# Performance work log

Hardware: AMD Instinct MI355X
Metric: run time of the kernel (lower is better)

## Reference

```python
import jax, jax.numpy as jnp
import numpy as np

N_NODES = 10000
N_EDGES = 160000
MUL0 = 128   # multiplicity of 0e in node input/output
MUL1 = 64    # multiplicity of 1o in node input/output
FC_IN = 8    # radial basis size (edge_scalar_attr dim)
FC_H = 64    # fc_neurons = [64, 64]
NUM_NEIGHBORS = 16.0
ANGLE = np.pi / 8.0
MID0 = MUL0 + MUL1   # 192 scalars in irreps_mid (simplified)
MID1 = MUL0 + MUL1   # 192 vectors (1o) in irreps_mid


def _inv_sqrt(d):
    return 1.0 / np.sqrt(d)


def setup_inputs() -> dict:
    key = jax.random.key(0)
    ks = jax.random.split(key, 18)
    rn = lambda k, shape: jax.random.normal(k, shape, dtype=jnp.float32)
    inp = {
        'node_input': rn(ks[0], (N_NODES, MUL0 + 3 * MUL1)),
        'edge_attr': rn(ks[1], (N_EDGES, 4)),            # 1x0e + 1x1o spherical harmonics
        'edge_scalar_attr': rn(ks[2], (N_EDGES, FC_IN)),
        # first Linear: node_input -> (node_features || node_self_out)
        'Wa0': rn(ks[3], (MUL0, MUL0)),   # 0e -> 0e (message branch)
        'Wa1': rn(ks[4], (MUL1, MUL1)),   # 1o -> 1o (message branch)
        'Wb0': rn(ks[5], (MUL0, MUL0)),   # 0e -> 0e (self branch)
        'Wb1': rn(ks[6], (MUL1, MUL1)),   # 1o -> 1o (self branch)
        # radial MLP
        'M1': rn(ks[7], (FC_IN, FC_H)),
        'M2': rn(ks[8], (FC_H, FC_H)),
        # per-instruction TP weight generators: [FC_H, mul] ('uvu', v=1 squeezed)
        'Wtp0': rn(ks[9], (FC_H, MUL0)),   # 0e x 0e -> 0e
        'Wtp1': rn(ks[10], (FC_H, MUL0)),  # 0e x 1o -> 1o
        'Wtp2': rn(ks[11], (FC_H, MUL1)),  # 1o x 0e -> 1o
        'Wtp3': rn(ks[12], (FC_H, MUL1)),  # 1o x 1o -> 0e
        # output Linear: irreps_mid (192x0e + 192x1o) -> 128x0e + 64x1o
        'Wo0': rn(ks[13], (MID0, MUL0)),
        'Wo1': rn(ks[14], (MID1, MUL1)),
        'edge_src': jax.random.randint(ks[15], (N_EDGES,), 0, N_NODES),
        'edge_dst': jax.random.randint(ks[16], (N_EDGES,), 0, N_NODES),
    }
    return inp


def _forward(node_input, edge_attr, edge_scalar_attr,
             Wa0, Wa1, Wb0, Wb1, M1, M2,
             Wtp0, Wtp1, Wtp2, Wtp3, Wo0, Wo1,
             edge_src, edge_dst):
    n = node_input.shape[0]
    x0 = node_input[:, :MUL0]                         # [N,128] 0e
    x1 = node_input[:, MUL0:].reshape(n, MUL1, 3)     # [N,64,3] 1o

    # Linear(node_input.irreps + irreps_node_output): split into message / self
    feat0 = (x0 @ Wa0) * _inv_sqrt(MUL0)
    feat1 = jnp.einsum('nvi,vu->nui', x1, Wa1) * _inv_sqrt(MUL1)
    self0 = (x0 @ Wb0) * _inv_sqrt(MUL0)
    self1 = jnp.einsum('nvi,vu->nui', x1, Wb1) * _inv_sqrt(MUL1)

    # gather node features to edges
    e0 = feat0[edge_src]                              # [E,128]
    e1 = feat1[edge_src]                              # [E,64,3]
    y0 = edge_attr[:, 0:1]                            # [E,1] 0e
    y1 = edge_attr[:, 1:4]                            # [E,3] 1o

    # radial MLP -> per-edge per-path 'uvu' weights (path param / sqrt(fc_out))
    h = jax.nn.gelu(edge_scalar_attr @ M1 * _inv_sqrt(FC_IN))
    h = jax.nn.gelu(h @ M2 * _inv_sqrt(FC_H))
    w0 = h @ Wtp0 * _inv_sqrt(FC_H)                   # [E,128]
    w1 = h @ Wtp1 * _inv_sqrt(FC_H)                   # [E,128]
    w2 = h @ Wtp2 * _inv_sqrt(FC_H)                   # [E,64]
    w3 = h @ Wtp3 * _inv_sqrt(FC_H)                   # [E,64]

    # CG tensor product paths (component normalization: alpha = sqrt(dim_out))
    mid0a = w0 * e0 * y0                                        # 0e x 0e -> 0e [E,128]
    mid0b = w3 * jnp.einsum('eui,ei->eu', e1, y1) * _inv_sqrt(3.0)  # 1o.1o -> 0e [E,64]
    mid1a = w1[:, :, None] * e0[:, :, None] * y1[:, None, :]   # 0e x 1o -> 1o [E,128,3]
    mid1b = w2[:, :, None] * e1 * y0[:, :, None]                # 1o x 0e -> 1o [E,64,3]

    e_cnt = edge_attr.shape[0]
    edge_mid = jnp.concatenate(
        [mid0a, mid0b, mid1a.reshape(e_cnt, -1), mid1b.reshape(e_cnt, -1)], axis=1)  # [E,768]

    # scatter-add to destination nodes, divide by sqrt(num_neighbors)
    agg = jax.ops.segment_sum(edge_mid, edge_dst, num_segments=n) * _inv_sqrt(NUM_NEIGHBORS)

    z0 = agg[:, :MID0]                                          # [N,192] 0e
    z1 = jnp.concatenate(
        [agg[:, MID0:MID0 + 3 * MUL0].reshape(n, MUL0, 3),
         agg[:, MID0 + 3 * MUL0:].reshape(n, MUL1, 3)], axis=1)  # [N,192,3] 1o

    conv0 = (z0 @ Wo0) * _inv_sqrt(MID0)
    conv1 = jnp.einsum('nvi,vu->nui', z1, Wo1) * _inv_sqrt(MID1)

    c = np.cos(ANGLE).astype(np.float32)
    s = np.sin(ANGLE).astype(np.float32)
    out0 = c * self0 + s * conv0                                 # [N,128]
    out1 = c * self1 + s * conv1                                 # [N,64,3]
    return jnp.concatenate([out0, out1.reshape(n, -1)], axis=1)  # [N,320]


def reference(node_input, edge_attr, edge_scalar_attr,
              Wa0, Wa1, Wb0, Wb1, M1, M2,
              Wtp0, Wtp1, Wtp2, Wtp3, Wo0, Wo1,
              edge_src, edge_dst):
    return _forward(node_input, edge_attr, edge_scalar_attr,
                    Wa0, Wa1, Wb0, Wb1, M1, M2,
                    Wtp0, Wtp1, Wtp2, Wtp3, Wo0, Wo1,
                    edge_src, edge_dst)
```

## Files before the change

### kernel.cpp

```cpp
#include <hip/hip_runtime.h>
#include <hip/hip_bf16.h>
#include <hip/hip_fp16.h>

#define N_NODES 10000
#define N_EDGES 160000
#define FEAT_W 320
#define CHUNK 32

typedef _Float16 half8 __attribute__((ext_vector_type(8)));
typedef float f32x4 __attribute__((ext_vector_type(4)));

__device__ __forceinline__ float gelu_tanh(float x) {
    float x3 = x * x * x;
    float t = tanhf(0.7978845608028654f * (x + 0.044715f * x3));
    return 0.5f * x * (1.0f + t);
}

__global__ __launch_bounds__(320) void node_transform(
    const float* __restrict__ node_input,
    const float* __restrict__ Wa0, const float* __restrict__ Wa1,
    const float* __restrict__ Wb0, const float* __restrict__ Wb1,
    float* __restrict__ feat_tbl, float* __restrict__ self_tbl)
{
    __shared__ __align__(16) float xT[FEAT_W][8];
    const int node0 = blockIdx.x * 8;
    const int t = threadIdx.x;
    for (int q = t; q < 640; q += 320) {
        const int n = q / 80, c4 = q - n * 80;
        const float4 v = ((const float4*)(node_input + (size_t)(node0 + n) * FEAT_W))[c4];
        xT[c4 * 4 + 0][n] = v.x; xT[c4 * 4 + 1][n] = v.y;
        xT[c4 * 4 + 2][n] = v.z; xT[c4 * 4 + 3][n] = v.w;
    }
    __syncthreads();

    float accf[8] = {0,0,0,0,0,0,0,0}, accs[8] = {0,0,0,0,0,0,0,0};
    float scale;
    if (t < 128) {
        for (int v = 0; v < 128; ++v) {
            const float wa = Wa0[v * 128 + t];
            const float wb = Wb0[v * 128 + t];
            const float4 xa = *(const float4*)&xT[v][0];
            const float4 xb = *(const float4*)&xT[v][4];
            accf[0] += xa.x * wa; accf[1] += xa.y * wa; accf[2] += xa.z * wa; accf[3] += xa.w * wa;
            accf[4] += xb.x * wa; accf[5] += xb.y * wa; accf[6] += xb.z * wa; accf[7] += xb.w * wa;
            accs[0] += xa.x * wb; accs[1] += xa.y * wb; accs[2] += xa.z * wb; accs[3] += xa.w * wb;
            accs[4] += xb.x * wb; accs[5] += xb.y * wb; accs[6] += xb.z * wb; accs[7] += xb.w * wb;
        }
        scale = 0.08838834764831845f;
    } else {
        const int r = t - 128, u = r / 3, i = r - 3 * u;
        for (int v = 0; v < 64; ++v) {
            const float wa = Wa1[v * 64 + u];
            const float wb = Wb1[v * 64 + u];
            const int row = 128 + v * 3 + i;
            const float4 xa = *(const float4*)&xT[row][0];
            const float4 xb = *(const float4*)&xT[row][4];
            accf[0] += xa.x * wa; accf[1] += xa.y * wa; accf[2] += xa.z * wa; accf[3] += xa.w * wa;
            accf[4] += xb.x * wa; accf[5] += xb.y * wa; accf[6] += xb.z * wa; accf[7] += xb.w * wa;
            accs[0] += xa.x * wb; accs[1] += xa.y * wb; accs[2] += xa.z * wb; accs[3] += xa.w * wb;
            accs[4] += xb.x * wb; accs[5] += xb.y * wb; accs[6] += xb.z * wb; accs[7] += xb.w * wb;
        }
        scale = 0.125f;
    }
#pragma unroll
    for (int n = 0; n < 8; ++n) {
        feat_tbl[(size_t)(node0 + n) * FEAT_W + t] = accf[n] * scale;
        self_tbl[(size_t)(node0 + n) * FEAT_W + t] = accs[n] * scale;
    }
}

__global__ __launch_bounds__(256) void mlp_kernel(
    const float* __restrict__ esa,
    const float* __restrict__ M1,
    const float* __restrict__ M2,
    const int* __restrict__ edge_dst,
    __half* __restrict__ h2buf,
    int* __restrict__ counts)
{
    __shared__ __align__(16) float sh[4][64];
    const int wave = threadIdx.x >> 6;
    const int lane = threadIdx.x & 63;
    const int e = blockIdx.x * 4 + wave;

    if (lane == 0) atomicAdd(&counts[edge_dst[e]], 1);

    const float4 e0 = ((const float4*)(esa + (size_t)e * 8))[0];
    const float4 e1 = ((const float4*)(esa + (size_t)e * 8))[1];
    float h = e0.x * M1[0 * 64 + lane] + e0.y * M1[1 * 64 + lane]
            + e0.z * M1[2 * 64 + lane] + e0.w * M1[3 * 64 + lane]
            + e1.x * M1[4 * 64 + lane] + e1.y * M1[5 * 64 + lane]
            + e1.z * M1[6 * 64 + lane] + e1.w * M1[7 * 64 + lane];
    h = gelu_tanh(h * 0.35355339059327373f);
    sh[wave][lane] = h;
    __syncthreads();

    float h2 = 0.f;
    const float4* shp = (const float4*)sh[wave];
#pragma unroll
    for (int q = 0; q < 16; ++q) {
        const float4 s = shp[q];
        h2 += s.x * M2[(4 * q + 0) * 64 + lane];
        h2 += s.y * M2[(4 * q + 1) * 64 + lane];
        h2 += s.z * M2[(4 * q + 2) * 64 + lane];
        h2 += s.w * M2[(4 * q + 3) * 64 + lane];
    }
    h2 = gelu_tanh(h2 * 0.125f);
    h2buf[(size_t)e * 64 + lane] = (__half)(h2 * 0.125f);
}

__global__ __launch_bounds__(256) void pack_wtp(
    const float* __restrict__ Wtp0, const float* __restrict__ Wtp1,
    const float* __restrict__ Wtp2, const float* __restrict__ Wtp3,
    __half* __restrict__ wtp_pack)
{
    const int gid = blockIdx.x * 256 + threadIdx.x;
    if (gid >= 24 * 64) return;
    const int lane = gid & 63;
    const int tile = gid >> 6;
    const int quad = lane >> 4, n16 = lane & 15;
    const int col = tile * 16 + n16;
    const float* src; int stride;
    if (col < 128)      { src = Wtp0 + col;         stride = 128; }
    else if (col < 256) { src = Wtp1 + (col - 128); stride = 128; }
    else if (col < 320) { src = Wtp2 + (col - 256); stride = 64;  }
    else                { src = Wtp3 + (col - 320); stride = 64;  }
    __half* dst = wtp_pack + (size_t)gid * 16;
#pragma unroll
    for (int s = 0; s < 2; ++s)
#pragma unroll
        for (int j = 0; j < 8; ++j)
            dst[s * 8 + j] = (__half)src[(s * 32 + quad * 8 + j) * stride];
}

__global__ __launch_bounds__(1024) void scan_kernel(
    const int* __restrict__ counts, int* __restrict__ offsets, int* __restrict__ cursor)
{
    __shared__ int wsum[16];
    const int wid = threadIdx.x >> 6, lane = threadIdx.x & 63;
    int base = 0;
    for (int c = 0; c < 10; ++c) {
        const int i = c * 1024 + threadIdx.x;
        const int v = (i < N_NODES) ? counts[i] : 0;
        int x = v;
#pragma unroll
        for (int off = 1; off < 64; off <<= 1) {
            int y = __shfl_up(x, off, 64);
            if (lane >= off) x += y;
        }
        if (lane == 63) wsum[wid] = x;
        __syncthreads();
        if (threadIdx.x < 16) {
            int s = wsum[threadIdx.x];
#pragma unroll
            for (int off = 1; off < 16; off <<= 1) {
                int y = __shfl_up(s, off, 64);
                if ((int)threadIdx.x >= off) s += y;
            }
            wsum[threadIdx.x] = s;
        }
        __syncthreads();
        const int waveoff = (wid == 0) ? 0 : wsum[wid - 1];
        const int excl = base + waveoff + x - v;
        if (i < N_NODES) { offsets[i] = excl; cursor[i] = excl; }
        const int tot = wsum[15];
        __syncthreads();
        base += tot;
    }
    if (threadIdx.x == 0) offsets[N_NODES] = base;
}

__global__ void fill_kernel(const int* __restrict__ edge_dst,
                            const int* __restrict__ edge_src,
                            const float* __restrict__ edge_attr,
                            int* __restrict__ cursor, int* __restrict__ elist,
                            int* __restrict__ srcs_csr, float* __restrict__ y4csr) {
    int e = blockIdx.x * 256 + threadIdx.x;
    if (e < N_EDGES) {
        int pos = atomicAdd(&cursor[edge_dst[e]], 1);
        elist[pos] = e;
        srcs_csr[pos] = edge_src[e];
        ((float4*)y4csr)[pos] = ((const float4*)edge_attr)[e];
    }
}

__global__ __launch_bounds__(384) void gather_kernel(
    const int* __restrict__ offsets,
    const int* __restrict__ elist,
    const int* __restrict__ srcs_csr,
    const float* __restrict__ y4csr,
    const __half* __restrict__ h2buf,
    const __half* __restrict__ wtp_pack,
    const float* __restrict__ feat_tbl,
    const float* __restrict__ self_tbl,
    const float* __restrict__ Wo0,
    const float* __restrict__ Wo1,
    float* __restrict__ out)
{
    __shared__ __align__(16) __half wsh[CHUNK * 384];
    __shared__ __align__(16) __half h2s[CHUNK * 64];
    __shared__ float ys[CHUNK][4];
    __shared__ int   srcs[CHUNK];
    __shared__ float z[768];

    const int node = blockIdx.x;
    const int t = threadIdx.x;
    const int wave = t >> 6, lane = t & 63;
    const int quad = lane >> 4, n16 = lane & 15;

    half8 bf[4][2];
#pragma unroll
    for (int c = 0; c < 4; ++c) {
        const __half* p = wtp_pack + (size_t)((wave * 4 + c) * 64 + lane) * 16;
        bf[c][0] = *(const half8*)p;
        bf[c][1] = *(const half8*)(p + 8);
    }

    int f0;
    if (t < 128)      f0 = t;
    else if (t < 256) f0 = t - 128;
    else if (t < 320) f0 = 128 + 3 * (t - 256);
    else              f0 = 128 + 3 * (t - 320);

    float acc = 0.f, acc3a = 0.f, acc3b = 0.f, acc3c = 0.f;
    const int beg = offsets[node], end = offsets[node + 1];

    for (int cb = beg; cb < end; cb += CHUNK) {
        const int ne = min(CHUNK, end - cb);
        if (t < ne) {
            srcs[t] = srcs_csr[cb + t];
            ((float4*)ys)[t] = ((const float4*)y4csr)[cb + t];
        }
        for (int q = t; q < ne * 8; q += 384) {
            const int eL = q >> 3, u = q & 7;
            const half8 hv = ((const half8*)(h2buf + (size_t)elist[cb + eL] * 64))[u];
            *(half8*)((char*)h2s + eL * 128 + ((u * 16) ^ ((eL & 7) << 4))) = hv;
        }
        __syncthreads();

#pragma unroll
        for (int g = 0; g < 2; ++g) {
            if (g * 16 < ne) {
                const int e = g * 16 + n16;
                const char* hb = (const char*)h2s + e * 128;
                const int sw = (e & 7) << 4;
                const half8 af0 = *(const half8*)(hb + ((quad * 16) ^ sw));
                const half8 af1 = *(const half8*)(hb + ((64 + quad * 16) ^ sw));
#pragma unroll
                for (int c = 0; c < 4; ++c) {
                    f32x4 acc4 = {0.f, 0.f, 0.f, 0.f};
                    acc4 = __builtin_amdgcn_mfma_f32_16x16x32_f16(af0, bf[c][0], acc4, 0, 0, 0);
                    acc4 = __builtin_amdgcn_mfma_f32_16x16x32_f16(af1, bf[c][1], acc4, 0, 0, 0);
                    const int col = (wave * 4 + c) * 16 + n16;
#pragma unroll
                    for (int r = 0; r < 4; ++r)
                        wsh[(g * 16 + quad * 4 + r) * 384 + col] = (__half)acc4[r];
                }
            }
        }
        __syncthreads();

        if (t < 128) {
            for (int e = 0; e < ne; ++e) {
                const float w = __half2float(wsh[e * 384 + t]);
                const float* fr = feat_tbl + (size_t)srcs[e] * FEAT_W;
                acc += w * fr[f0] * ys[e][0];
            }
        } else if (t < 256) {
            for (int e = 0; e < ne; ++e) {
                const float w = __half2float(wsh[e * 384 + t]);
                const float* fr = feat_tbl + (size_t)srcs[e] * FEAT_W;
                const float p = w * fr[f0];
                acc3a += p * ys[e][1];
                acc3b += p * ys[e][2];
                acc3c += p * ys[e][3];
            }
        } else if (t < 320) {
            for (int e = 0; e < ne; ++e) {
                const float w = __half2float(wsh[e * 384 + t]);
                const float* fr = feat_tbl + (size_t)srcs[e] * FEAT_W;
                const float p = w * ys[e][0];
                acc3a += p * fr[f0];
                acc3b += p * fr[f0 + 1];
                acc3c += p * fr[f0 + 2];
            }
        } else {
            for (int e = 0; e < ne; ++e) {
                const float w = __half2float(wsh[e * 384 + t]);
                const float* fr = feat_tbl + (size_t)srcs[e] * FEAT_W;
                const float d = fr[f0] * ys[e][1] + fr[f0 + 1] * ys[e][2]
                              + fr[f0 + 2] * ys[e][3];
                acc += w * d;
            }
        }
        __syncthreads();
    }

    const float sZ = 0.25f;
    if (t < 128) {
        z[t] = acc * sZ;
    } else if (t < 256) {
        const int u = t - 128;
        z[192 + 0 * 192 + u] = acc3a * sZ;
        z[192 + 1 * 192 + u] = acc3b * sZ;
        z[192 + 2 * 192 + u] = acc3c * sZ;
    } else if (t < 320) {
        const int u = t - 256;
        z[192 + 0 * 192 + 128 + u] = acc3a * sZ;
        z[192 + 1 * 192 + 128 + u] = acc3b * sZ;
        z[192 + 2 * 192 + 128 + u] = acc3c * sZ;
    } else {
        z[128 + (t - 320)] = acc * sZ * 0.5773502691896258f;
    }
    __syncthreads();

    const float sA = 0.07216878364870323f;
    const float cR = 0.92387953251128674f;
    const float sR = 0.38268343236508978f;

    if (t < 128) {
        float conv = 0.f;
        const float4* z4 = (const float4*)z;
#pragma unroll 8
        for (int q = 0; q < 48; ++q) {
            const float4 zz = z4[q];
            conv += zz.x * Wo0[(4 * q + 0) * 128 + t];
            conv += zz.y * Wo0[(4 * q + 1) * 128 + t];
            conv += zz.z * Wo0[(4 * q + 2) * 128 + t];
            conv += zz.w * Wo0[(4 * q + 3) * 128 + t];
        }
        const float sv = self_tbl[(size_t)node * FEAT_W + t];
        out[(size_t)node * FEAT_W + t] = cR * sv + sR * conv * sA;
    } else if (t < 320) {
        const int idx = t - 128;
        const int i = idx >> 6, u = idx & 63;
        float conv = 0.f;
        const float4* z4 = (const float4*)(z + 192 + i * 192);
#pragma unroll 8
        for (int q = 0; q < 48; ++q) {
            const float4 zz = z4[q];
            conv += zz.x * Wo1[(4 * q + 0) * 64 + u];
            conv += zz.y * Wo1[(4 * q + 1) * 64 + u];
            conv += zz.z * Wo1[(4 * q + 2) * 64 + u];
            conv += zz.w * Wo1[(4 * q + 3) * 64 + u];
        }
        const int col = 128 + u * 3 + i;
        const float sv = self_tbl[(size_t)node * FEAT_W + col];
        out[(size_t)node * FEAT_W + col] = cR * sv + sR * conv * sA;
    }
}

extern "C" void kernel_launch(void* const* d_in, const int* in_sizes, int n_in,
                              void* d_out, int out_size, void* d_ws, size_t ws_size,
                              hipStream_t stream) {
    const float* node_input = (const float*)d_in[0];
    const float* edge_attr  = (const float*)d_in[1];
    const float* esa        = (const float*)d_in[2];
    const float* Wa0  = (const float*)d_in[3];
    const float* Wa1  = (const float*)d_in[4];
    const float* Wb0  = (const float*)d_in[5];
    const float* Wb1  = (const float*)d_in[6];
    const float* M1   = (const float*)d_in[7];
    const float* M2   = (const float*)d_in[8];
    const float* Wtp0 = (const float*)d_in[9];
    const float* Wtp1 = (const float*)d_in[10];
    const float* Wtp2 = (const float*)d_in[11];
    const float* Wtp3 = (const float*)d_in[12];
    const float* Wo0  = (const float*)d_in[13];
    const float* Wo1  = (const float*)d_in[14];
    const int* edge_src = (const int*)d_in[15];
    const int* edge_dst = (const int*)d_in[16];
    float* out = (float*)d_out;

    float*  feat_tbl = (float*)d_ws;
    float*  self_tbl = feat_tbl + (size_t)N_NODES * FEAT_W;
    __half* h2buf    = (__half*)(self_tbl + (size_t)N_NODES * FEAT_W);
    float*  y4csr    = (float*)(h2buf + (size_t)N_EDGES * 64);
    int*    counts   = (int*)(y4csr + (size_t)N_EDGES * 4);
    int*    offsets  = counts + N_NODES;
    int*    cursor   = offsets + N_NODES + 1;
    int*    elist    = cursor + N_NODES;
    int*    srcs_csr = elist + N_EDGES;
    __half* wtp_pack = (__half*)(srcs_csr + N_EDGES);

    hipMemsetAsync(counts, 0, sizeof(int) * N_NODES, stream);

    pack_wtp<<<6, 256, 0, stream>>>(Wtp0, Wtp1, Wtp2, Wtp3, wtp_pack);
    node_transform<<<N_NODES / 8, 320, 0, stream>>>(node_input, Wa0, Wa1, Wb0, Wb1,
                                                    feat_tbl, self_tbl);
    mlp_kernel<<<N_EDGES / 4, 256, 0, stream>>>(esa, M1, M2, edge_dst, h2buf, counts);
    scan_kernel<<<1, 1024, 0, stream>>>(counts, offsets, cursor);
    fill_kernel<<<N_EDGES / 256, 256, 0, stream>>>(edge_dst, edge_src, edge_attr,
                                                   cursor, elist, srcs_csr, y4csr);
    gather_kernel<<<N_NODES, 384, 0, stream>>>(offsets, elist, srcs_csr, y4csr,
                                               h2buf, wtp_pack, feat_tbl, self_tbl,
                                               Wo0, Wo1, out);
}
```

Measured before the change: 407.2 us.

## Build CSR before MLP, write h2 in CSR order, prefetch chunks in gather

Edge counting, scan and fill now run before the radial MLP, which writes its fp16 outputs directly at each edge's CSR position. The gather kernel can then read contiguous h2 rows instead of going through an indirect elist lookup. Gather also register-prefetches the next chunk while the current one computes, reuses one shared buffer for h2s and z, XOR-swizzles the wsh shared layout to cut bank conflicts, and sets an occupancy hint. Wo0/Wo1 are packed to fp16 to halve weight traffic in the output projection, at some precision cost and with an extra count kernel launch.

```diff
diff --git a/kernel.cpp b/kernel.cpp
--- a/kernel.cpp
+++ b/kernel.cpp
@@ -69,20 +69,78 @@
     }
 }
 
+__global__ __launch_bounds__(256) void count_kernel(
+    const int* __restrict__ edge_dst, int* __restrict__ counts)
+{
+    const int e = blockIdx.x * 256 + threadIdx.x;
+    if (e < N_EDGES) atomicAdd(&counts[edge_dst[e]], 1);
+}
+
+__global__ __launch_bounds__(1024) void scan_kernel(
+    const int* __restrict__ counts, int* __restrict__ offsets, int* __restrict__ cursor)
+{
+    __shared__ int wsum[16];
+    const int wid = threadIdx.x >> 6, lane = threadIdx.x & 63;
+    int base = 0;
+    for (int c = 0; c < 10; ++c) {
+        const int i = c * 1024 + threadIdx.x;
+        const int v = (i < N_NODES) ? counts[i] : 0;
+        int x = v;
+#pragma unroll
+        for (int off = 1; off < 64; off <<= 1) {
+            int y = __shfl_up(x, off, 64);
+            if (lane >= off) x += y;
+        }
+        if (lane == 63) wsum[wid] = x;
+        __syncthreads();
+        if (threadIdx.x < 16) {
+            int s = wsum[threadIdx.x];
+#pragma unroll
+            for (int off = 1; off < 16; off <<= 1) {
+                int y = __shfl_up(s, off, 64);
+                if ((int)threadIdx.x >= off) s += y;
+            }
+            wsum[threadIdx.x] = s;
+        }
+        __syncthreads();
+        const int waveoff = (wid == 0) ? 0 : wsum[wid - 1];
+        const int excl = base + waveoff + x - v;
+        if (i < N_NODES) { offsets[i] = excl; cursor[i] = excl; }
+        const int tot = wsum[15];
+        __syncthreads();
+        base += tot;
+    }
+    if (threadIdx.x == 0) offsets[N_NODES] = base;
+}
+
+__global__ void fill_kernel(const int* __restrict__ edge_dst,
+                            const int* __restrict__ edge_src,
+                            const float* __restrict__ edge_attr,
+                            int* __restrict__ cursor,
+                            int* __restrict__ srcs_csr, float* __restrict__ y4csr,
+                            int* __restrict__ pos_csr) {
+    int e = blockIdx.x * 256 + threadIdx.x;
+    if (e < N_EDGES) {
+        int pos = atomicAdd(&cursor[edge_dst[e]], 1);
+        srcs_csr[pos] = edge_src[e];
+        ((float4*)y4csr)[pos] = ((const float4*)edge_attr)[e];
+        pos_csr[e] = pos;
+    }
+}
+
 __global__ __launch_bounds__(256) void mlp_kernel(
     const float* __restrict__ esa,
     const float* __restrict__ M1,
     const float* __restrict__ M2,
-    const int* __restrict__ edge_dst,
-    __half* __restrict__ h2buf,
-    int* __restrict__ counts)
+    const int* __restrict__ pos_csr,
+    __half* __restrict__ h2csr)
 {
     __shared__ __align__(16) float sh[4][64];
     const int wave = threadIdx.x >> 6;
     const int lane = threadIdx.x & 63;
     const int e = blockIdx.x * 4 + wave;
 
-    if (lane == 0) atomicAdd(&counts[edge_dst[e]], 1);
+    const int pos = pos_csr[e];
 
     const float4 e0 = ((const float4*)(esa + (size_t)e * 8))[0];
     const float4 e1 = ((const float4*)(esa + (size_t)e * 8))[1];
@@ -105,107 +163,71 @@
         h2 += s.w * M2[(4 * q + 3) * 64 + lane];
     }
     h2 = gelu_tanh(h2 * 0.125f);
-    h2buf[(size_t)e * 64 + lane] = (__half)(h2 * 0.125f);
-}
-
-__global__ __launch_bounds__(256) void pack_wtp(
+    h2csr[(size_t)pos * 64 + lane] = (__half)(h2 * 0.125f);
+}
+
+__global__ __launch_bounds__(256) void pack_weights(
     const float* __restrict__ Wtp0, const float* __restrict__ Wtp1,
     const float* __restrict__ Wtp2, const float* __restrict__ Wtp3,
-    __half* __restrict__ wtp_pack)
+    const float* __restrict__ Wo0,  const float* __restrict__ Wo1,
+    __half* __restrict__ wtp_pack, __half* __restrict__ wo_pack)
 {
     const int gid = blockIdx.x * 256 + threadIdx.x;
-    if (gid >= 24 * 64) return;
-    const int lane = gid & 63;
-    const int tile = gid >> 6;
-    const int quad = lane >> 4, n16 = lane & 15;
-    const int col = tile * 16 + n16;
-    const float* src; int stride;
-    if (col < 128)      { src = Wtp0 + col;         stride = 128; }
-    else if (col < 256) { src = Wtp1 + (col - 128); stride = 128; }
-    else if (col < 320) { src = Wtp2 + (col - 256); stride = 64;  }
-    else                { src = Wtp3 + (col - 320); stride = 64;  }
-    __half* dst = wtp_pack + (size_t)gid * 16;
-#pragma unroll
-    for (int s = 0; s < 2; ++s)
-#pragma unroll
-        for (int j = 0; j < 8; ++j)
-            dst[s * 8 + j] = (__half)src[(s * 32 + quad * 8 + j) * stride];
-}
-
-__global__ __launch_bounds__(1024) void scan_kernel(
-    const int* __restrict__ counts, int* __restrict__ offsets, int* __restrict__ cursor)
-{
-    __shared__ int wsum[16];
-    const int wid = threadIdx.x >> 6, lane = threadIdx.x & 63;
-    int base = 0;
-    for (int c = 0; c < 10; ++c) {
-        const int i = c * 1024 + threadIdx.x;
-        const int v = (i < N_NODES) ? counts[i] : 0;
-        int x = v;
-#pragma unroll
-        for (int off = 1; off < 64; off <<= 1) {
-            int y = __shfl_up(x, off, 64);
-            if (lane >= off) x += y;
-        }
-        if (lane == 63) wsum[wid] = x;
-        __syncthreads();
-        if (threadIdx.x < 16) {
-            int s = wsum[threadIdx.x];
-#pragma unroll
-            for (int off = 1; off < 16; off <<= 1) {
-                int y = __shfl_up(s, off, 64);
-                if ((int)threadIdx.x >= off) s += y;
-            }
-            wsum[threadIdx.x] = s;
-        }
-        __syncthreads();
-        const int waveoff = (wid == 0) ? 0 : wsum[wid - 1];
-        const int excl = base + waveoff + x - v;
-        if (i < N_NODES) { offsets[i] = excl; cursor[i] = excl; }
-        const int tot = wsum[15];
-        __syncthreads();
-        base += tot;
-    }
-    if (threadIdx.x == 0) offsets[N_NODES] = base;
-}
-
-__global__ void fill_kernel(const int* __restrict__ edge_dst,
-                            const int* __restrict__ edge_src,
-                            const float* __restrict__ edge_attr,
-                            int* __restrict__ cursor, int* __restrict__ elist,
-                            int* __restrict__ srcs_csr, float* __restrict__ y4csr) {
-    int e = blockIdx.x * 256 + threadIdx.x;
-    if (e < N_EDGES) {
-        int pos = atomicAdd(&cursor[edge_dst[e]], 1);
-        elist[pos] = e;
-        srcs_csr[pos] = edge_src[e];
-        ((float4*)y4csr)[pos] = ((const float4*)edge_attr)[e];
-    }
-}
-
-__global__ __launch_bounds__(384) void gather_kernel(
+    if (gid < 1536) {
+        const int lane = gid & 63;
+        const int tile = gid >> 6;
+        const int quad = lane >> 4, n16 = lane & 15;
+        const int col = tile * 16 + n16;
+        const float* src; int stride;
+        if (col < 128)      { src = Wtp0 + col;         stride = 128; }
+        else if (col < 256) { src = Wtp1 + (col - 128); stride = 128; }
+        else if (col < 320) { src = Wtp2 + (col - 256); stride = 64;  }
+        else                { src = Wtp3 + (col - 320); stride = 64;  }
+        __half* dst = wtp_pack + (size_t)gid * 16;
+#pragma unroll
+        for (int s = 0; s < 2; ++s)
+#pragma unroll
+            for (int j = 0; j < 8; ++j)
+                dst[s * 8 + j] = (__half)src[(s * 32 + quad * 8 + j) * stride];
+    } else {
+        const int i = gid - 1536;
+        if (i < 24576) wo_pack[i] = (__half)Wo0[i];
+        else           wo_pack[i] = (__half)Wo1[i - 24576];
+    }
+}
+
+__global__ __launch_bounds__(384, 7) void gather_kernel(
     const int* __restrict__ offsets,
-    const int* __restrict__ elist,
     const int* __restrict__ srcs_csr,
     const float* __restrict__ y4csr,
-    const __half* __restrict__ h2buf,
+    const __half* __restrict__ h2csr,
     const __half* __restrict__ wtp_pack,
     const float* __restrict__ feat_tbl,
     const float* __restrict__ self_tbl,
-    const float* __restrict__ Wo0,
-    const float* __restrict__ Wo1,
+    const __half* __restrict__ wo_pack,
     float* __restrict__ out)
 {
     __shared__ __align__(16) __half wsh[CHUNK * 384];
-    __shared__ __align__(16) __half h2s[CHUNK * 64];
+    __shared__ __align__(16) char pool[CHUNK * 128];
     __shared__ float ys[CHUNK][4];
     __shared__ int   srcs[CHUNK];
-    __shared__ float z[768];
+    __half* h2s = (__half*)pool;
+    float*  z   = (float*)pool;
 
     const int node = blockIdx.x;
     const int t = threadIdx.x;
     const int wave = t >> 6, lane = t & 63;
     const int quad = lane >> 4, n16 = lane & 15;
+
+    const int beg = offsets[node], end = offsets[node + 1];
+
+    int cb = beg;
+    int ne = min(CHUNK, end - cb);
+    half8 hreg = {};
+    int   sreg = 0;
+    float4 yreg = {0.f, 0.f, 0.f, 0.f};
+    if (t < ne * 8) hreg = ((const half8*)(h2csr + (size_t)cb * 64))[t];
+    if (t < ne)     { sreg = srcs_csr[cb + t]; yreg = ((const float4*)y4csr)[cb + t]; }
 
     half8 bf[4][2];
 #pragma unroll
@@ -222,18 +244,12 @@
     else              f0 = 128 + 3 * (t - 320);
 
     float acc = 0.f, acc3a = 0.f, acc3b = 0.f, acc3c = 0.f;
-    const int beg = offsets[node], end = offsets[node + 1];
-
-    for (int cb = beg; cb < end; cb += CHUNK) {
-        const int ne = min(CHUNK, end - cb);
-        if (t < ne) {
-            srcs[t] = srcs_csr[cb + t];
-            ((float4*)ys)[t] = ((const float4*)y4csr)[cb + t];
-        }
-        for (int q = t; q < ne * 8; q += 384) {
-            const int eL = q >> 3, u = q & 7;
-            const half8 hv = ((const half8*)(h2buf + (size_t)elist[cb + eL] * 64))[u];
-            *(half8*)((char*)h2s + eL * 128 + ((u * 16) ^ ((eL & 7) << 4))) = hv;
+
+    for (;;) {
+        if (t < ne) { srcs[t] = sreg; ((float4*)ys)[t] = yreg; }
+        if (t < ne * 8) {
+            const int eL = t >> 3, u = t & 7;
+            *(half8*)((char*)h2s + eL * 128 + ((u * 16) ^ ((eL & 7) << 4))) = hreg;
         }
         __syncthreads();
 
@@ -250,24 +266,35 @@
                     f32x4 acc4 = {0.f, 0.f, 0.f, 0.f};
                     acc4 = __builtin_amdgcn_mfma_f32_16x16x32_f16(af0, bf[c][0], acc4, 0, 0, 0);
                     acc4 = __builtin_amdgcn_mfma_f32_16x16x32_f16(af1, bf[c][1], acc4, 0, 0, 0);
-                    const int col = (wave * 4 + c) * 16 + n16;
-#pragma unroll
-                    for (int r = 0; r < 4; ++r)
-                        wsh[(g * 16 + quad * 4 + r) * 384 + col] = (__half)acc4[r];
+                    const int colb = ((wave * 4 + c) * 16 + n16) * 2;
+#pragma unroll
+                    for (int r = 0; r < 4; ++r) {
+                        const int row = g * 16 + quad * 4 + r;
+                        *(__half*)((char*)wsh + row * 768 + (colb ^ (quad << 5))) =
+                            (__half)acc4[r];
+                    }
                 }
             }
         }
-        __syncthreads();
-
+
+        const int cb2 = cb + CHUNK;
+        const int ne2 = (cb2 < end) ? min(CHUNK, end - cb2) : 0;
+        if (t < ne2 * 8) hreg = ((const half8*)(h2csr + (size_t)cb2 * 64))[t];
+        if (t < ne2)     { sreg = srcs_csr[cb2 + t]; yreg = ((const float4*)y4csr)[cb2 + t]; }
+        __syncthreads();
+
+        const int tb = t * 2;
         if (t < 128) {
             for (int e = 0; e < ne; ++e) {
-                const float w = __half2float(wsh[e * 384 + t]);
+                const float w = __half2float(*(const __half*)(
+                    (const char*)wsh + e * 768 + (tb ^ (((e >> 2) & 3) << 5))));
                 const float* fr = feat_tbl + (size_t)srcs[e] * FEAT_W;
                 acc += w * fr[f0] * ys[e][0];
             }
         } else if (t < 256) {
             for (int e = 0; e < ne; ++e) {
-                const float w = __half2float(wsh[e * 384 + t]);
+                const float w = __half2float(*(const __half*)(
+                    (const char*)wsh + e * 768 + (tb ^ (((e >> 2) & 3) << 5))));
                 const float* fr = feat_tbl + (size_t)srcs[e] * FEAT_W;
                 const float p = w * fr[f0];
                 acc3a += p * ys[e][1];
@@ -276,7 +303,8 @@
             }
         } else if (t < 320) {
             for (int e = 0; e < ne; ++e) {
-                const float w = __half2float(wsh[e * 384 + t]);
+                const float w = __half2float(*(const __half*)(
+                    (const char*)wsh + e * 768 + (tb ^ (((e >> 2) & 3) << 5))));
                 const float* fr = feat_tbl + (size_t)srcs[e] * FEAT_W;
                 const float p = w * ys[e][0];
                 acc3a += p * fr[f0];
@@ -285,13 +313,17 @@
             }
         } else {
             for (int e = 0; e < ne; ++e) {
-                const float w = __half2float(wsh[e * 384 + t]);
+                const float w = __half2float(*(const __half*)(
+                    (const char*)wsh + e * 768 + (tb ^ (((e >> 2) & 3) << 5))));
                 const float* fr = feat_tbl + (size_t)srcs[e] * FEAT_W;
                 const float d = fr[f0] * ys[e][1] + fr[f0 + 1] * ys[e][2]
                               + fr[f0 + 2] * ys[e][3];
                 acc += w * d;
             }
         }
+
+        if (!ne2) break;
+        cb = cb2; ne = ne2;
         __syncthreads();
     }
 
@@ -316,6 +348,8 @@
     const float sA = 0.07216878364870323f;
     const float cR = 0.92387953251128674f;
     const float sR = 0.38268343236508978f;
+    const __half* Wo0h = wo_pack;
+    const __half* Wo1h = wo_pack + 24576;
 
     if (t < 128) {
         float conv = 0.f;
@@ -323,10 +357,10 @@
 #pragma unroll 8
         for (int q = 0; q < 48; ++q) {
             const float4 zz = z4[q];
-            conv += zz.x * Wo0[(4 * q + 0) * 128 + t];
-            conv += zz.y * Wo0[(4 * q + 1) * 128 + t];
-            conv += zz.z * Wo0[(4 * q + 2) * 128 + t];
-            conv += zz.w * Wo0[(4 * q + 3) * 128 + t];
+            conv += zz.x * (float)Wo0h[(4 * q + 0) * 128 + t];
+            conv += zz.y * (float)Wo0h[(4 * q + 1) * 128 + t];
+            conv += zz.z * (float)Wo0h[(4 * q + 2) * 128 + t];
+            conv += zz.w * (float)Wo0h[(4 * q + 3) * 128 + t];
         }
         const float sv = self_tbl[(size_t)node * FEAT_W + t];
         out[(size_t)node * FEAT_W + t] = cR * sv + sR * conv * sA;
@@ -338,10 +372,10 @@
 #pragma unroll 8
         for (int q = 0; q < 48; ++q) {
             const float4 zz = z4[q];
-            conv += zz.x * Wo1[(4 * q + 0) * 64 + u];
-            conv += zz.y * Wo1[(4 * q + 1) * 64 + u];
-            conv += zz.z * Wo1[(4 * q + 2) * 64 + u];
-            conv += zz.w * Wo1[(4 * q + 3) * 64 + u];
+            conv += zz.x * (float)Wo1h[(4 * q + 0) * 64 + u];
+            conv += zz.y * (float)Wo1h[(4 * q + 1) * 64 + u];
+            conv += zz.z * (float)Wo1h[(4 * q + 2) * 64 + u];
+            conv += zz.w * (float)Wo1h[(4 * q + 3) * 64 + u];
         }
         const int col = 128 + u * 3 + i;
         const float sv = self_tbl[(size_t)node * FEAT_W + col];
@@ -371,27 +405,31 @@
     const int* edge_dst = (const int*)d_in[16];
     float* out = (float*)d_out;
 
-    float*  feat_tbl = (float*)d_ws;
-    float*  self_tbl = feat_tbl + (size_t)N_NODES * FEAT_W;
-    __half* h2buf    = (__half*)(self_tbl + (size_t)N_NODES * FEAT_W);
-    float*  y4csr    = (float*)(h2buf + (size_t)N_EDGES * 64);
-    int*    counts   = (int*)(y4csr + (size_t)N_EDGES * 4);
-    int*    offsets  = counts + N_NODES;
-    int*    cursor   = offsets + N_NODES + 1;
-    int*    elist    = cursor + N_NODES;
-    int*    srcs_csr = elist + N_EDGES;
-    __half* wtp_pack = (__half*)(srcs_csr + N_EDGES);
+    char* w = (char*)d_ws;
+    float*  feat_tbl = (float*)w;           w += (size_t)N_NODES * FEAT_W * 4;
+    float*  self_tbl = (float*)w;           w += (size_t)N_NODES * FEAT_W * 4;
+    float*  y4csr    = (float*)w;           w += (size_t)N_EDGES * 4 * 4;
+    __half* h2csr    = (__half*)w;          w += (size_t)N_EDGES * 64 * 2;
+    __half* wtp_pack = (__half*)w;          w += (size_t)24576 * 2;
+    __half* wo_pack  = (__half*)w;          w += (size_t)36864 * 2;
+    int*    counts   = (int*)w;             w += (size_t)N_NODES * 4;
+    int*    offsets  = (int*)w;             w += (size_t)(N_NODES + 1) * 4;
+    int*    cursor   = (int*)w;             w += (size_t)N_NODES * 4;
+    int*    srcs_csr = (int*)w;             w += (size_t)N_EDGES * 4;
+    int*    pos_csr  = (int*)w;             w += (size_t)N_EDGES * 4;
 
     hipMemsetAsync(counts, 0, sizeof(int) * N_NODES, stream);
 
-    pack_wtp<<<6, 256, 0, stream>>>(Wtp0, Wtp1, Wtp2, Wtp3, wtp_pack);
+    count_kernel<<<N_EDGES / 256, 256, 0, stream>>>(edge_dst, counts);
+    scan_kernel<<<1, 1024, 0, stream>>>(counts, offsets, cursor);
+    fill_kernel<<<N_EDGES / 256, 256, 0, stream>>>(edge_dst, edge_src, edge_attr,
+                                                   cursor, srcs_csr, y4csr, pos_csr);
+    pack_weights<<<150, 256, 0, stream>>>(Wtp0, Wtp1, Wtp2, Wtp3, Wo0, Wo1,
+                                          wtp_pack, wo_pack);
     node_transform<<<N_NODES / 8, 320, 0, stream>>>(node_input, Wa0, Wa1, Wb0, Wb1,
                                                     feat_tbl, self_tbl);
-    mlp_kernel<<<N_EDGES / 4, 256, 0, stream>>>(esa, M1, M2, edge_dst, h2buf, counts);
-    scan_kernel<<<1, 1024, 0, stream>>>(counts, offsets, cursor);
-    fill_kernel<<<N_EDGES / 256, 256, 0, stream>>>(edge_dst, edge_src, edge_attr,
-                                                   cursor, elist, srcs_csr, y4csr);
-    gather_kernel<<<N_NODES, 384, 0, stream>>>(offsets, elist, srcs_csr, y4csr,
-                                               h2buf, wtp_pack, feat_tbl, self_tbl,
-                                               Wo0, Wo1, out);
-}
+    mlp_kernel<<<N_EDGES / 4, 256, 0, stream>>>(esa, M1, M2, pos_csr, h2csr);
+    gather_kernel<<<N_NODES, 384, 0, stream>>>(offsets, srcs_csr, y4csr, h2csr,
+                                               wtp_pack, feat_tbl, self_tbl,
+                                               wo_pack, out);
+}
```

Measured after the change: 426.0 us. 4.6% more time.
